# Optimization experiments

Hardware: AMD Instinct MI355X
Metric: run time of the kernel (lower is better)

Reference implementation:

```python
import math
import jax, jax.numpy as jnp
import numpy as np

HID = 256; NH = 8; DH = 32; DFF = 1024  # int(4.0*256)
N = 10000; E = 160000; NV = 128; NG = 64


def _ln(x, eps=1e-6):
    m = jnp.mean(x, axis=-1, keepdims=True)
    v = jnp.mean((x - m) ** 2, axis=-1, keepdims=True)
    return (x - m) * jax.lax.rsqrt(v + eps)


def _modulate(x, shift, scale):
    return x * (1.0 + scale) + shift


def _swiglu(x, W12, Wout):
    a, b = jnp.split(x @ W12, 2, axis=-1)
    return (jax.nn.silu(a) * b) @ Wout


def _adaln(t, W, b):
    return jnp.split(jax.nn.silu(t) @ W + b, 6, axis=-1)


def setup_inputs() -> dict:
    key = jax.random.key(0)
    ks = jax.random.split(key, 32)
    rn = lambda k, shape, s=1.0: jax.random.normal(k, shape, jnp.float32) * s
    W = 0.02
    return {
        "batch": jnp.sort(jax.random.randint(ks[0], (N,), 0, NG)),
        "x": rn(ks[1], (N, HID)),
        "t_emb_h": rn(ks[2], (N, HID)),
        "edge_attr": rn(ks[3], (E, HID)),
        "edge_index": jax.random.randint(ks[4], (2, E), 0, N),
        "t_emb_e": rn(ks[5], (E, HID)),
        "dist": rn(ks[6], (E, NV)),
        "W_edge_emb": rn(ks[7], (HID + NV, HID), W),
        "b_edge_emb": jnp.zeros((HID,), jnp.float32),
        "W_adaln": rn(ks[8], (HID, 6 * HID), W),
        "b_adaln": jnp.zeros((6 * HID,), jnp.float32),
        "W_adaln_e": rn(ks[9], (HID, 6 * HID), W),
        "b_adaln_e": jnp.zeros((6 * HID,), jnp.float32),
        "W_qkv": rn(ks[10], (HID, 3 * HID), W),
        "W_e0": rn(ks[11], (HID, HID), W),
        "W_e1": rn(ks[12], (HID, HID), W),
        "W_n2e": rn(ks[13], (HID, HID), W),
        "b_n2e": jnp.zeros((HID,), jnp.float32),
        "g_ln": jnp.ones((HID,), jnp.float32),
        "b_ln": jnp.zeros((HID,), jnp.float32),
        "W_ffn12": rn(ks[14], (HID, 2 * DFF), W),
        "W_ffn_out": rn(ks[15], (DFF, HID), W),
        "W_ffne12": rn(ks[16], (HID, 2 * DFF), W),
        "W_ffne_out": rn(ks[17], (DFF, HID), W),
    }


def reference(batch, x, t_emb_h, edge_attr, edge_index, t_emb_e, dist,
              W_edge_emb, b_edge_emb, W_adaln, b_adaln, W_adaln_e, b_adaln_e,
              W_qkv, W_e0, W_e1, W_n2e, b_n2e, g_ln, b_ln,
              W_ffn12, W_ffn_out, W_ffne12, W_ffne_out):
    src, tgt = edge_index[0], edge_index[1]
    n = x.shape[0]
    h_in_node = x
    h_in_edge = edge_attr

    shift_msa, scale_msa, gate_msa, shift_mlp, scale_mlp, gate_mlp = _adaln(t_emb_h, W_adaln, b_adaln)
    e_shift_msa, e_scale_msa, e_gate_msa, e_shift_mlp, e_scale_mlp, e_gate_mlp = _adaln(t_emb_e, W_adaln_e, b_adaln_e)

    edge_attr_e = jnp.concatenate([edge_attr, dist], axis=-1) @ W_edge_emb + b_edge_emb
    x_mod = _modulate(_ln(x), shift_msa, scale_msa)
    prev_edge_attr = edge_attr_e
    e_mod = _modulate(_ln(edge_attr_e), e_shift_msa, e_scale_msa)

    qkv = x_mod @ W_qkv                         # N x 3H
    Q, K, V = jnp.split(qkv, 3, axis=-1)
    Q = Q.reshape(-1, NH, DH)
    K = K.reshape(-1, NH, DH)
    V = V.reshape(-1, NH, DH)

    query_i = Q[src]                            # E x NH x DH
    key_j = K[tgt]
    value_j = V[tgt]
    edge_attn = jax.nn.gelu(e_mod @ W_e0, approximate=True).reshape(-1, NH, DH)

    alpha = jnp.sum(query_i * key_j * edge_attn, axis=-1) / math.sqrt(DH)  # E x NH
    # segment softmax over edges grouped by target node
    amax = jax.ops.segment_max(alpha, tgt, num_segments=n)                 # N x NH
    exp_a = jnp.exp(alpha - amax[tgt])
    denom = jax.ops.segment_sum(exp_a, tgt, num_segments=n)
    alpha = exp_a / denom[tgt]

    msg = value_j * (e_mod @ W_e1).reshape(-1, NH, DH) * alpha[..., None]
    out = jax.ops.segment_sum(msg.reshape(-1, NH * DH), tgt, num_segments=n)  # N x H

    h_node = out
    h_edge = (h_node[src] + h_node[tgt]) @ W_n2e + b_n2e

    h_node = h_in_node + gate_msa * h_node
    h_node = _modulate(_ln(h_node) * g_ln + b_ln, shift_mlp, scale_mlp)
    h_out = h_node + gate_mlp * _swiglu(h_node, W_ffn12, W_ffn_out)

    h_edge = h_in_edge + e_gate_msa * h_edge
    h_edge = _modulate(_ln(h_edge), e_shift_mlp, e_scale_mlp)
    h_edge_out = prev_edge_attr + h_edge + e_gate_mlp * _swiglu(h_edge, W_ffne12, W_ffne_out)
    return (h_out, h_edge_out)
```

## Files before the change

### kernel.cpp

```cpp
#include <hip/hip_runtime.h>

#define HID 256

typedef unsigned short u16;
typedef __attribute__((ext_vector_type(8))) short bf16x8;
typedef __attribute__((ext_vector_type(4))) float f32x4;

__device__ __forceinline__ float siluf(float x) { return x / (1.f + __expf(-x)); }
__device__ __forceinline__ float geluf(float x) {
    return x / (1.f + __expf(-(1.59576912f * x + 0.07135481f * x * x * x)));
}
__device__ __forceinline__ u16 f2b(float x) {
    unsigned u = __float_as_uint(x);
    unsigned r = u + 0x7FFFu + ((u >> 16) & 1u);
    return (u16)(r >> 16);
}
__device__ __forceinline__ float b2f(u16 h) {
    return __uint_as_float(((unsigned)h) << 16);
}
__device__ __forceinline__ void gload16(const u16* g, u16* l) {
    __builtin_amdgcn_global_load_lds(
        (const __attribute__((address_space(1))) unsigned int*)g,
        (__attribute__((address_space(3))) unsigned int*)l, 16, 0, 0);
}
__device__ __forceinline__ int imin(int a, int b) { return a < b ? a : b; }

union B16x8 { u16 u[8]; uint4 q; };

__global__ __launch_bounds__(256) void gemm_mfma(
    const u16* __restrict__ A, int lda,
    const u16* __restrict__ Bt, int ldb,
    void* __restrict__ Cv, int ldc,
    int M, int N, int K,
    const float* __restrict__ bias, int act, int obf16)
{
    __shared__ u16 lds[8192];

    const int tid  = threadIdx.x;
    const int lane = tid & 63;
    const int wave = tid >> 6;
    const int row0 = blockIdx.y * 64;
    const int col0 = blockIdx.x * 128;
    const int wm   = (wave >> 1) * 32;
    const int wn   = (wave & 1) * 64;

    f32x4 acc[2][4];
#pragma unroll
    for (int i = 0; i < 2; ++i)
#pragma unroll
        for (int j = 0; j < 4; ++j) acc[i][j] = (f32x4)0.0f;

    const int kc = (lane & 3) * 8;
    const int rr  = wave * 16 + (lane >> 2);
    const int rb1 = (wave + 4) * 16 + (lane >> 2);
    const u16* pa  = A + (size_t)imin(row0 + rr, M - 1) * lda + kc;
    const u16* pb0 = Bt + (size_t)(col0 + rr) * ldb + kc;
    const u16* pb1 = Bt + (size_t)(col0 + rb1) * ldb + kc;
    u16* la  = &lds[wave * 512];
    u16* lb0 = &lds[2048 + wave * 512];
    u16* lb1 = &lds[2048 + (wave + 4) * 512];

    const int kb = (lane >> 4) * 8;
    const int fr = lane & 15;

    for (int k0 = 0; k0 < K; k0 += 32) {
        gload16(pa + k0, la);
        gload16(pb0 + k0, lb0);
        gload16(pb1 + k0, lb1);
        __syncthreads();

        bf16x8 af[2], bfm[4];
#pragma unroll
        for (int i = 0; i < 2; ++i)
            af[i] = *(const bf16x8*)&lds[(wm + i * 16 + fr) * 32 + kb];
#pragma unroll
        for (int j = 0; j < 4; ++j)
            bfm[j] = *(const bf16x8*)&lds[2048 + (wn + j * 16 + fr) * 32 + kb];
#pragma unroll
        for (int i = 0; i < 2; ++i)
#pragma unroll
            for (int j = 0; j < 4; ++j)
                acc[i][j] = __builtin_amdgcn_mfma_f32_16x16x32_bf16(af[i], bfm[j], acc[i][j], 0, 0, 0);
        __syncthreads();
    }

    const int qr = (lane >> 4) * 4;
    if (obf16) {
#pragma unroll
        for (int i = 0; i < 2; ++i)
#pragma unroll
            for (int r = 0; r < 4; ++r)
#pragma unroll
                for (int j = 0; j < 4; ++j) {
                    int lcol = wn + j * 16 + fr;
                    int gcol = col0 + lcol;
                    float v = acc[i][j][r];
                    if (bias) v += bias[gcol];
                    if (act == 2) v = geluf(v);
                    else if (act == 1) v = siluf(v);
                    lds[(wm + i * 16 + qr + r) * 128 + lcol] = f2b(v);
                }
        __syncthreads();
        int row = tid >> 2, cc0 = (tid & 3) * 32;
        int grow = row0 + row;
        if (grow < M) {
            uint4* dst = (uint4*)((u16*)Cv + (size_t)grow * ldc + col0 + cc0);
            const uint4* sp = (const uint4*)&lds[row * 128 + cc0];
            dst[0] = sp[0]; dst[1] = sp[1]; dst[2] = sp[2]; dst[3] = sp[3];
        }
    } else {
        float* Cf = (float*)Cv;
#pragma unroll
        for (int i = 0; i < 2; ++i)
#pragma unroll
            for (int r = 0; r < 4; ++r) {
                int grow = row0 + wm + i * 16 + qr + r;
                if (grow >= M) continue;
#pragma unroll
                for (int j = 0; j < 4; ++j) {
                    int gcol = col0 + wn + j * 16 + fr;
                    float v = acc[i][j][r];
                    if (bias) v += bias[gcol];
                    if (act == 2) v = geluf(v);
                    else if (act == 1) v = siluf(v);
                    Cf[(size_t)grow * ldc + gcol] = v;
                }
            }
    }
}

__global__ __launch_bounds__(256) void gemm_e01(
    const u16* __restrict__ A, const u16* __restrict__ Bt,
    u16* __restrict__ e1b, int M,
    const u16* __restrict__ qkv, const int* __restrict__ srcI, const int* __restrict__ tgtI,
    float* __restrict__ alpha)
{
    __shared__ u16 lds[8192];

    const int tid  = threadIdx.x;
    const int lane = tid & 63;
    const int wave = tid >> 6;
    const int row0 = blockIdx.y * 64;
    const int bx   = blockIdx.x;
    const int col0 = bx * 128;
    const int wm   = (wave >> 1) * 32;
    const int wn   = (wave & 1) * 64;

    f32x4 acc[2][4];
#pragma unroll
    for (int i = 0; i < 2; ++i)
#pragma unroll
        for (int j = 0; j < 4; ++j) acc[i][j] = (f32x4)0.0f;

    const int kc = (lane & 3) * 8;
    const int rr  = wave * 16 + (lane >> 2);
    const int rb1 = (wave + 4) * 16 + (lane >> 2);
    const u16* pa  = A + (size_t)imin(row0 + rr, M - 1) * 256 + kc;
    const u16* pb0 = Bt + (size_t)(col0 + rr) * 256 + kc;
    const u16* pb1 = Bt + (size_t)(col0 + rb1) * 256 + kc;
    u16* la  = &lds[wave * 512];
    u16* lb0 = &lds[2048 + wave * 512];
    u16* lb1 = &lds[2048 + (wave + 4) * 512];

    const int kb = (lane >> 4) * 8;
    const int fr = lane & 15;

    for (int k0 = 0; k0 < 256; k0 += 32) {
        gload16(pa + k0, la);
        gload16(pb0 + k0, lb0);
        gload16(pb1 + k0, lb1);
        __syncthreads();

        bf16x8 af[2], bfm[4];
#pragma unroll
        for (int i = 0; i < 2; ++i)
            af[i] = *(const bf16x8*)&lds[(wm + i * 16 + fr) * 32 + kb];
#pragma unroll
        for (int j = 0; j < 4; ++j)
            bfm[j] = *(const bf16x8*)&lds[2048 + (wn + j * 16 + fr) * 32 + kb];
#pragma unroll
        for (int i = 0; i < 2; ++i)
#pragma unroll
            for (int j = 0; j < 4; ++j)
                acc[i][j] = __builtin_amdgcn_mfma_f32_16x16x32_bf16(af[i], bfm[j], acc[i][j], 0, 0, 0);
        __syncthreads();
    }

    const int qr = (lane >> 4) * 4;
    const bool isE0 = (bx < 2);
#pragma unroll
    for (int i = 0; i < 2; ++i)
#pragma unroll
        for (int r = 0; r < 4; ++r)
#pragma unroll
            for (int j = 0; j < 4; ++j) {
                int lcol = wn + j * 16 + fr;
                float v = acc[i][j][r];
                if (isE0) v = geluf(v);
                lds[(wm + i * 16 + qr + r) * 128 + lcol] = f2b(v);
            }
    __syncthreads();
    int row = tid >> 2, cc0 = (tid & 3) * 32;
    int grow = row0 + row;
    if (grow < M) {
        if (isE0) {
            int head = bx * 4 + (tid & 3);
            const u16* qv = qkv + (size_t)srcI[grow] * 768 + head * 32;
            const u16* kv = qkv + (size_t)tgtI[grow] * 768 + 256 + head * 32;
            const u16* gv = &lds[row * 128 + cc0];
            float s = 0.f;
#pragma unroll
            for (int c = 0; c < 32; ++c)
                s += b2f(gv[c]) * b2f(qv[c]) * b2f(kv[c]);
            alpha[(size_t)grow * 8 + head] = s * 0.17677669529663687f;
        } else {
            uint4* dst = (uint4*)(e1b + (size_t)grow * 256 + (col0 - 256) + cc0);
            const uint4* sp = (const uint4*)&lds[row * 128 + cc0];
            dst[0] = sp[0]; dst[1] = sp[1]; dst[2] = sp[2]; dst[3] = sp[3];
        }
    }
}

__global__ __launch_bounds__(256) void gemm_cat(
    const float* __restrict__ A1, const float* __restrict__ A2,
    const u16* __restrict__ Bt,
    u16* __restrict__ C, int M, const float* __restrict__ bias)
{
    __shared__ u16 lds[8192];

    const int tid  = threadIdx.x;
    const int lane = tid & 63;
    const int wave = tid >> 6;
    const int row0 = blockIdx.y * 64;
    const int col0 = blockIdx.x * 128;
    const int wm   = (wave >> 1) * 32;
    const int wn   = (wave & 1) * 64;

    f32x4 acc[2][4];
#pragma unroll
    for (int i = 0; i < 2; ++i)
#pragma unroll
        for (int j = 0; j < 4; ++j) acc[i][j] = (f32x4)0.0f;

    const int kc = (lane & 3) * 8;
    const int rr  = wave * 16 + (lane >> 2);
    const int rb1 = (wave + 4) * 16 + (lane >> 2);
    const int gr  = imin(row0 + rr, M - 1);
    const u16* pb0 = Bt + (size_t)(col0 + rr) * 384 + kc;
    const u16* pb1 = Bt + (size_t)(col0 + rb1) * 384 + kc;
    u16* lb0 = &lds[2048 + wave * 512];
    u16* lb1 = &lds[2048 + (wave + 4) * 512];
    u16* laD = &lds[wave * 512 + (lane & 63) * 8];

    const int kb = (lane >> 4) * 8;
    const int fr = lane & 15;

    for (int k0 = 0; k0 < 384; k0 += 32) {
        int kk = k0 + kc;
        const float* sp = (kk < 256) ? (A1 + (size_t)gr * 256 + kk)
                                     : (A2 + (size_t)gr * 128 + (kk - 256));
        float4 v0 = *(const float4*)sp;
        float4 v1 = *(const float4*)(sp + 4);
        gload16(pb0 + k0, lb0);
        gload16(pb1 + k0, lb1);
        B16x8 t;
        t.u[0] = f2b(v0.x); t.u[1] = f2b(v0.y); t.u[2] = f2b(v0.z); t.u[3] = f2b(v0.w);
        t.u[4] = f2b(v1.x); t.u[5] = f2b(v1.y); t.u[6] = f2b(v1.z); t.u[7] = f2b(v1.w);
        *(uint4*)laD = t.q;
        __syncthreads();

        bf16x8 af[2], bfm[4];
#pragma unroll
        for (int i = 0; i < 2; ++i)
            af[i] = *(const bf16x8*)&lds[(wm + i * 16 + fr) * 32 + kb];
#pragma unroll
        for (int j = 0; j < 4; ++j)
            bfm[j] = *(const bf16x8*)&lds[2048 + (wn + j * 16 + fr) * 32 + kb];
#pragma unroll
        for (int i = 0; i < 2; ++i)
#pragma unroll
            for (int j = 0; j < 4; ++j)
                acc[i][j] = __builtin_amdgcn_mfma_f32_16x16x32_bf16(af[i], bfm[j], acc[i][j], 0, 0, 0);
        __syncthreads();
    }

    const int qr = (lane >> 4) * 4;
#pragma unroll
    for (int i = 0; i < 2; ++i)
#pragma unroll
        for (int r = 0; r < 4; ++r)
#pragma unroll
            for (int j = 0; j < 4; ++j) {
                int lcol = wn + j * 16 + fr;
                float v = acc[i][j][r] + bias[col0 + lcol];
                lds[(wm + i * 16 + qr + r) * 128 + lcol] = f2b(v);
            }
    __syncthreads();
    int row = tid >> 2, cc0 = (tid & 3) * 32;
    int grow = row0 + row;
    if (grow < M) {
        uint4* dst = (uint4*)(C + (size_t)grow * 256 + col0 + cc0);
        const uint4* sp = (const uint4*)&lds[row * 128 + cc0];
        dst[0] = sp[0]; dst[1] = sp[1]; dst[2] = sp[2]; dst[3] = sp[3];
    }
}

__global__ __launch_bounds__(256) void gemm_gsum(
    const float* __restrict__ hat, const int* __restrict__ srcI, const int* __restrict__ tgtI,
    const u16* __restrict__ Bt,
    u16* __restrict__ C, int M, const float* __restrict__ bias)
{
    __shared__ u16 lds[8192];

    const int tid  = threadIdx.x;
    const int lane = tid & 63;
    const int wave = tid >> 6;
    const int row0 = blockIdx.y * 64;
    const int col0 = blockIdx.x * 128;
    const int wm   = (wave >> 1) * 32;
    const int wn   = (wave & 1) * 64;

    f32x4 acc[2][4];
#pragma unroll
    for (int i = 0; i < 2; ++i)
#pragma unroll
        for (int j = 0; j < 4; ++j) acc[i][j] = (f32x4)0.0f;

    const int kc = (lane & 3) * 8;
    const int rr  = wave * 16 + (lane >> 2);
    const int rb1 = (wave + 4) * 16 + (lane >> 2);
    const int gr  = imin(row0 + rr, M - 1);
    const float* ps = hat + (size_t)srcI[gr] * 256 + kc;
    const float* pt = hat + (size_t)tgtI[gr] * 256 + kc;
    const u16* pb0 = Bt + (size_t)(col0 + rr) * 256 + kc;
    const u16* pb1 = Bt + (size_t)(col0 + rb1) * 256 + kc;
    u16* lb0 = &lds[2048 + wave * 512];
    u16* lb1 = &lds[2048 + (wave + 4) * 512];
    u16* laD = &lds[wave * 512 + (lane & 63) * 8];

    const int kb = (lane >> 4) * 8;
    const int fr = lane & 15;

    for (int k0 = 0; k0 < 256; k0 += 32) {
        float4 a0 = *(const float4*)(ps + k0);
        float4 a1 = *(const float4*)(ps + k0 + 4);
        float4 b0 = *(const float4*)(pt + k0);
        float4 b1 = *(const float4*)(pt + k0 + 4);
        gload16(pb0 + k0, lb0);
        gload16(pb1 + k0, lb1);
        B16x8 t;
        t.u[0] = f2b(a0.x + b0.x); t.u[1] = f2b(a0.y + b0.y);
        t.u[2] = f2b(a0.z + b0.z); t.u[3] = f2b(a0.w + b0.w);
        t.u[4] = f2b(a1.x + b1.x); t.u[5] = f2b(a1.y + b1.y);
        t.u[6] = f2b(a1.z + b1.z); t.u[7] = f2b(a1.w + b1.w);
        *(uint4*)laD = t.q;
        __syncthreads();

        bf16x8 af[2], bfm[4];
#pragma unroll
        for (int i = 0; i < 2; ++i)
            af[i] = *(const bf16x8*)&lds[(wm + i * 16 + fr) * 32 + kb];
#pragma unroll
        for (int j = 0; j < 4; ++j)
            bfm[j] = *(const bf16x8*)&lds[2048 + (wn + j * 16 + fr) * 32 + kb];
#pragma unroll
        for (int i = 0; i < 2; ++i)
#pragma unroll
            for (int j = 0; j < 4; ++j)
                acc[i][j] = __builtin_amdgcn_mfma_f32_16x16x32_bf16(af[i], bfm[j], acc[i][j], 0, 0, 0);
        __syncthreads();
    }

    const int qr = (lane >> 4) * 4;
#pragma unroll
    for (int i = 0; i < 2; ++i)
#pragma unroll
        for (int r = 0; r < 4; ++r)
#pragma unroll
            for (int j = 0; j < 4; ++j) {
                int lcol = wn + j * 16 + fr;
                float v = acc[i][j][r] + bias[col0 + lcol];
                lds[(wm + i * 16 + qr + r) * 128 + lcol] = f2b(v);
            }
    __syncthreads();
    int row = tid >> 2, cc0 = (tid & 3) * 32;
    int grow = row0 + row;
    if (grow < M) {
        uint4* dst = (uint4*)(C + (size_t)grow * 256 + col0 + cc0);
        const uint4* sp = (const uint4*)&lds[row * 128 + cc0];
        dst[0] = sp[0]; dst[1] = sp[1]; dst[2] = sp[2]; dst[3] = sp[3];
    }
}

__global__ __launch_bounds__(256) void gemm_ffn12(
    const u16* __restrict__ A, const u16* __restrict__ Wt,
    u16* __restrict__ C, int M)
{
    __shared__ u16 sm[6144];
    u16* lsA = sm;
    u16* lsB1 = sm + 2048;
    u16* lsB2 = sm + 4096;

    const int tid  = threadIdx.x;
    const int lane = tid & 63;
    const int wave = tid >> 6;
    const int row0 = blockIdx.y * 64;
    const int col0 = blockIdx.x * 64;
    const int wm   = (wave >> 1) * 32;
    const int wn   = (wave & 1) * 32;

    f32x4 accA[2][2], accB[2][2];
#pragma unroll
    for (int i = 0; i < 2; ++i)
#pragma unroll
        for (int j = 0; j < 2; ++j) { accA[i][j] = (f32x4)0.0f; accB[i][j] = (f32x4)0.0f; }

    const int kc = (lane & 3) * 8;
    const int rr = wave * 16 + (lane >> 2);
    const u16* pa  = A + (size_t)imin(row0 + rr, M - 1) * 256 + kc;
    const u16* pb1 = Wt + (size_t)(col0 + rr) * 256 + kc;
    const u16* pb2 = Wt + (size_t)(1024 + col0 + rr) * 256 + kc;
    u16* la  = &lsA[wave * 512];
    u16* lb1 = &lsB1[wave * 512];
    u16* lb2 = &lsB2[wave * 512];

    const int kb = (lane >> 4) * 8;
    const int fr = lane & 15;

#pragma unroll 1
    for (int k0 = 0; k0 < 256; k0 += 32) {
        gload16(pa + k0, la);
        gload16(pb1 + k0, lb1);
        gload16(pb2 + k0, lb2);
        __syncthreads();

        bf16x8 af[2], b1f[2], b2f_[2];
#pragma unroll
        for (int i = 0; i < 2; ++i)
            af[i] = *(const bf16x8*)&lsA[(wm + i * 16 + fr) * 32 + kb];
#pragma unroll
        for (int j = 0; j < 2; ++j) {
            b1f[j] = *(const bf16x8*)&lsB1[(wn + j * 16 + fr) * 32 + kb];
            b2f_[j] = *(const bf16x8*)&lsB2[(wn + j * 16 + fr) * 32 + kb];
        }
#pragma unroll
        for (int i = 0; i < 2; ++i)
#pragma unroll
            for (int j = 0; j < 2; ++j) {
                accA[i][j] = __builtin_amdgcn_mfma_f32_16x16x32_bf16(af[i], b1f[j], accA[i][j], 0, 0, 0);
                accB[i][j] = __builtin_amdgcn_mfma_f32_16x16x32_bf16(af[i], b2f_[j], accB[i][j], 0, 0, 0);
            }
        __syncthreads();
    }

    const int qr = (lane >> 4) * 4;
#pragma unroll
    for (int i = 0; i < 2; ++i)
#pragma unroll
        for (int r = 0; r < 4; ++r)
#pragma unroll
            for (int j = 0; j < 2; ++j) {
                float a = accA[i][j][r], b = accB[i][j][r];
                sm[(wm + i * 16 + qr + r) * 64 + wn + j * 16 + fr] = f2b(siluf(a) * b);
            }
    __syncthreads();
    int row = tid >> 2, cc0 = (tid & 3) * 16;
    int grow = row0 + row;
    if (grow < M) {
        uint4* dst = (uint4*)(C + (size_t)grow * 1024 + col0 + cc0);
        const uint4* sp = (const uint4*)&sm[row * 64 + cc0];
        dst[0] = sp[0]; dst[1] = sp[1];
    }
}

__global__ __launch_bounds__(256) void gemm_out_final(
    const u16* __restrict__ A, const u16* __restrict__ Bt,
    const u16* __restrict__ eae, const u16* __restrict__ h2,
    const u16* __restrict__ gate, int ldg, int goff,
    float* __restrict__ out, int M)
{
    __shared__ u16 lds[6144];

    const int tid  = threadIdx.x;
    const int lane = tid & 63;
    const int wave = tid >> 6;
    const int row0 = blockIdx.y * 64;
    const int col0 = blockIdx.x * 128;
    const int wm   = (wave >> 1) * 32;
    const int wn   = (wave & 1) * 64;

    f32x4 acc[2][4];
#pragma unroll
    for (int i = 0; i < 2; ++i)
#pragma unroll
        for (int j = 0; j < 4; ++j) acc[i][j] = (f32x4)0.0f;

    const int kc = (lane & 3) * 8;
    const int rr = wave * 16 + (lane >> 2);
    const int rb1 = (wave + 4) * 16 + (lane >> 2);
    const u16* pa  = A + (size_t)imin(row0 + rr, M - 1) * 1024 + kc;
    const u16* pb0 = Bt + (size_t)(col0 + rr) * 1024 + kc;
    const u16* pb1 = Bt + (size_t)(col0 + rb1) * 1024 + kc;
    u16* la  = &lds[wave * 512];
    u16* lb0 = &lds[2048 + wave * 512];
    u16* lb1 = &lds[2048 + (wave + 4) * 512];

    const int kb = (lane >> 4) * 8;
    const int fr = lane & 15;

#pragma unroll 1
    for (int k0 = 0; k0 < 1024; k0 += 32) {
        gload16(pa + k0, la);
        gload16(pb0 + k0, lb0);
        gload16(pb1 + k0, lb1);
        __syncthreads();

        bf16x8 af[2], bfm[4];
#pragma unroll
        for (int i = 0; i < 2; ++i)
            af[i] = *(const bf16x8*)&lds[(wm + i * 16 + fr) * 32 + kb];
#pragma unroll
        for (int j = 0; j < 4; ++j)
            bfm[j] = *(const bf16x8*)&lds[2048 + (wn + j * 16 + fr) * 32 + kb];
#pragma unroll
        for (int i = 0; i < 2; ++i)
#pragma unroll
            for (int j = 0; j < 4; ++j)
                acc[i][j] = __builtin_amdgcn_mfma_f32_16x16x32_bf16(af[i], bfm[j], acc[i][j], 0, 0, 0);
        __syncthreads();
    }

    const int qr = (lane >> 4) * 4;
#pragma unroll
    for (int i = 0; i < 2; ++i)
#pragma unroll
        for (int r = 0; r < 4; ++r) {
            int grow = row0 + wm + i * 16 + qr + r;
            if (grow >= M) continue;
#pragma unroll
            for (int j = 0; j < 4; ++j) {
                int gcol = col0 + wn + j * 16 + fr;
                size_t idx = (size_t)grow * 256 + gcol;
                float v = acc[i][j][r] * b2f(gate[(size_t)grow * ldg + goff + gcol]) + b2f(h2[idx]);
                if (eae) v += b2f(eae[idx]);
                out[idx] = v;
            }
        }
}

__global__ __launch_bounds__(256) void k_wconv(
    const float* __restrict__ W, u16* __restrict__ Wt, int K, int N)
{
    int i = blockIdx.x * 256 + threadIdx.x;
    if (i >= K * N) return;
    int n = i / K, k = i - n * K;
    Wt[i] = f2b(W[(size_t)k * N + n]);
}

__global__ __launch_bounds__(256) void k_silu_b16(
    const float* __restrict__ src, u16* __restrict__ dst, long long n4)
{
    long long i = (long long)blockIdx.x * 256 + threadIdx.x;
    if (i >= n4) return;
    float4 v = ((const float4*)src)[i];
    ushort4 o;
    o.x = f2b(siluf(v.x)); o.y = f2b(siluf(v.y)); o.z = f2b(siluf(v.z)); o.w = f2b(siluf(v.w));
    ((ushort4*)dst)[i] = o;
}

__global__ __launch_bounds__(256) void k_ln_mod_b16(
    const float* __restrict__ X, u16* __restrict__ Y, int M,
    const u16* __restrict__ ssb, int ldss, int shoff, int scoff)
{
    int row = (blockIdx.x << 2) + (threadIdx.x >> 6);
    if (row >= M) return;
    int lane = threadIdx.x & 63;
    const float* xr = X + (size_t)row * HID + lane * 4;
    float x0 = xr[0], x1 = xr[1], x2 = xr[2], x3 = xr[3];
    float s = x0 + x1 + x2 + x3;
    float q = x0 * x0 + x1 * x1 + x2 * x2 + x3 * x3;
#pragma unroll
    for (int o = 32; o; o >>= 1) { s += __shfl_xor(s, o, 64); q += __shfl_xor(q, o, 64); }
    float m = s * (1.f / HID);
    float r = rsqrtf(q * (1.f / HID) - m * m + 1e-6f);
    const u16* sp = ssb + (size_t)row * ldss;
    ushort4 sh = *(const ushort4*)(sp + shoff + lane * 4);
    ushort4 sc = *(const ushort4*)(sp + scoff + lane * 4);
    ushort4 o;
    o.x = f2b((x0 - m) * r * (1.f + b2f(sc.x)) + b2f(sh.x));
    o.y = f2b((x1 - m) * r * (1.f + b2f(sc.y)) + b2f(sh.y));
    o.z = f2b((x2 - m) * r * (1.f + b2f(sc.z)) + b2f(sh.z));
    o.w = f2b((x3 - m) * r * (1.f + b2f(sc.w)) + b2f(sh.w));
    ((ushort4*)(Y + (size_t)row * HID))[lane] = o;
}

__global__ __launch_bounds__(256) void k_ln_mod_b16src(
    const u16* __restrict__ X, u16* __restrict__ Y, int M,
    const u16* __restrict__ ssb, int ldss, int shoff, int scoff)
{
    int row = (blockIdx.x << 2) + (threadIdx.x >> 6);
    if (row >= M) return;
    int lane = threadIdx.x & 63;
    ushort4 xv = ((const ushort4*)(X + (size_t)row * HID))[lane];
    float x0 = b2f(xv.x), x1 = b2f(xv.y), x2 = b2f(xv.z), x3 = b2f(xv.w);
    float s = x0 + x1 + x2 + x3;
    float q = x0 * x0 + x1 * x1 + x2 * x2 + x3 * x3;
#pragma unroll
    for (int o = 32; o; o >>= 1) { s += __shfl_xor(s, o, 64); q += __shfl_xor(q, o, 64); }
    float m = s * (1.f / HID);
    float r = rsqrtf(q * (1.f / HID) - m * m + 1e-6f);
    const u16* sp = ssb + (size_t)row * ldss;
    ushort4 sh = *(const ushort4*)(sp + shoff + lane * 4);
    ushort4 sc = *(const ushort4*)(sp + scoff + lane * 4);
    ushort4 o;
    o.x = f2b((x0 - m) * r * (1.f + b2f(sc.x)) + b2f(sh.x));
    o.y = f2b((x1 - m) * r * (1.f + b2f(sc.y)) + b2f(sh.y));
    o.z = f2b((x2 - m) * r * (1.f + b2f(sc.z)) + b2f(sh.z));
    o.w = f2b((x3 - m) * r * (1.f + b2f(sc.w)) + b2f(sh.w));
    ((ushort4*)(Y + (size_t)row * HID))[lane] = o;
}

__global__ __launch_bounds__(256) void k_ln_mod_resid_b16(
    const float* __restrict__ A, const float* __restrict__ Bv, u16* __restrict__ Y, int M,
    const u16* __restrict__ gb, int ldg, int goff,
    const u16* __restrict__ ssb, int ldss, int shoff, int scoff,
    const float* __restrict__ gw, const float* __restrict__ bw)
{
    int row = (blockIdx.x << 2) + (threadIdx.x >> 6);
    if (row >= M) return;
    int lane = threadIdx.x & 63;
    const float* ar = A + (size_t)row * HID + lane * 4;
    const float* br = Bv + (size_t)row * HID + lane * 4;
    ushort4 gp = *(const ushort4*)(gb + (size_t)row * ldg + goff + lane * 4);
    float t0 = ar[0] + b2f(gp.x) * br[0];
    float t1 = ar[1] + b2f(gp.y) * br[1];
    float t2 = ar[2] + b2f(gp.z) * br[2];
    float t3 = ar[3] + b2f(gp.w) * br[3];
    float s = t0 + t1 + t2 + t3;
    float q = t0 * t0 + t1 * t1 + t2 * t2 + t3 * t3;
#pragma unroll
    for (int o = 32; o; o >>= 1) { s += __shfl_xor(s, o, 64); q += __shfl_xor(q, o, 64); }
    float m = s * (1.f / HID);
    float r = rsqrtf(q * (1.f / HID) - m * m + 1e-6f);
    float n0 = (t0 - m) * r, n1 = (t1 - m) * r, n2 = (t2 - m) * r, n3 = (t3 - m) * r;
    if (gw) {
        const float* g4 = gw + lane * 4;
        const float* b4 = bw + lane * 4;
        n0 = n0 * g4[0] + b4[0]; n1 = n1 * g4[1] + b4[1];
        n2 = n2 * g4[2] + b4[2]; n3 = n3 * g4[3] + b4[3];
    }
    const u16* sp = ssb + (size_t)row * ldss;
    ushort4 sh = *(const ushort4*)(sp + shoff + lane * 4);
    ushort4 sc = *(const ushort4*)(sp + scoff + lane * 4);
    ushort4 o;
    o.x = f2b(n0 * (1.f + b2f(sc.x)) + b2f(sh.x));
    o.y = f2b(n1 * (1.f + b2f(sc.y)) + b2f(sh.y));
    o.z = f2b(n2 * (1.f + b2f(sc.z)) + b2f(sh.z));
    o.w = f2b(n3 * (1.f + b2f(sc.w)) + b2f(sh.w));
    ((ushort4*)(Y + (size_t)row * HID))[lane] = o;
}

__global__ __launch_bounds__(256) void k_ln_mod_resid_b16bv(
    const float* __restrict__ A, const u16* __restrict__ Bv, u16* __restrict__ Y, int M,
    const u16* __restrict__ gb, int ldg, int goff,
    const u16* __restrict__ ssb, int ldss, int shoff, int scoff)
{
    int row = (blockIdx.x << 2) + (threadIdx.x >> 6);
    if (row >= M) return;
    int lane = threadIdx.x & 63;
    const float* ar = A + (size_t)row * HID + lane * 4;
    ushort4 bv = ((const ushort4*)(Bv + (size_t)row * HID))[lane];
    ushort4 gp = *(const ushort4*)(gb + (size_t)row * ldg + goff + lane * 4);
    float t0 = ar[0] + b2f(gp.x) * b2f(bv.x);
    float t1 = ar[1] + b2f(gp.y) * b2f(bv.y);
    float t2 = ar[2] + b2f(gp.z) * b2f(bv.z);
    float t3 = ar[3] + b2f(gp.w) * b2f(bv.w);
    float s = t0 + t1 + t2 + t3;
    float q = t0 * t0 + t1 * t1 + t2 * t2 + t3 * t3;
#pragma unroll
    for (int o = 32; o; o >>= 1) { s += __shfl_xor(s, o, 64); q += __shfl_xor(q, o, 64); }
    float m = s * (1.f / HID);
    float r = rsqrtf(q * (1.f / HID) - m * m + 1e-6f);
    float n0 = (t0 - m) * r, n1 = (t1 - m) * r, n2 = (t2 - m) * r, n3 = (t3 - m) * r;
    const u16* sp = ssb + (size_t)row * ldss;
    ushort4 sh = *(const ushort4*)(sp + shoff + lane * 4);
    ushort4 sc = *(const ushort4*)(sp + scoff + lane * 4);
    ushort4 o;
    o.x = f2b(n0 * (1.f + b2f(sc.x)) + b2f(sh.x));
    o.y = f2b(n1 * (1.f + b2f(sc.y)) + b2f(sh.y));
    o.z = f2b(n2 * (1.f + b2f(sc.z)) + b2f(sh.z));
    o.w = f2b(n3 * (1.f + b2f(sc.w)) + b2f(sh.w));
    ((ushort4*)(Y + (size_t)row * HID))[lane] = o;
}

__global__ __launch_bounds__(256) void k_hist(
    const int* __restrict__ tgt, int* __restrict__ counts, int E)
{
    int i = blockIdx.x * 256 + threadIdx.x;
    if (i < E) atomicAdd(&counts[tgt[i]], 1);
}

__global__ __launch_bounds__(256) void k_scan(
    const int* __restrict__ counts, int* __restrict__ offsets, int Nn)
{
    __shared__ int part[256];
    __shared__ int pref[257];
    int t = threadIdx.x;
    int chunk = (Nn + 255) / 256;
    int lo = t * chunk, hi = imin(lo + chunk, Nn);
    int s = 0;
    for (int i = lo; i < hi; ++i) s += counts[i];
    part[t] = s;
    __syncthreads();
    if (t == 0) {
        int run = 0;
        for (int i = 0; i < 256; ++i) { pref[i] = run; run += part[i]; }
        pref[256] = run;
        offsets[Nn] = run;
    }
    __syncthreads();
    int run = pref[t];
    for (int i = lo; i < hi; ++i) { offsets[i] = run; run += counts[i]; }
}

__global__ __launch_bounds__(256) void k_scatter(
    const int* __restrict__ tgt, int* __restrict__ cursor,
    int* __restrict__ eidlist, int E)
{
    int i = blockIdx.x * 256 + threadIdx.x;
    if (i < E) {
        int pos = atomicAdd(&cursor[tgt[i]], 1);
        eidlist[pos] = i;
    }
}

__global__ __launch_bounds__(256) void k_amax_den(
    const float* __restrict__ alpha, const int* __restrict__ offsets,
    const int* __restrict__ eidlist, float* __restrict__ amaxF,
    float* __restrict__ invden, int NH8)
{
    int i = blockIdx.x * 256 + threadIdx.x;
    if (i >= NH8) return;
    int n = i >> 3, h = i & 7;
    int b = offsets[n], e = offsets[n + 1];
    float m = -1e30f;
    for (int k = b; k < e; ++k) m = fmaxf(m, alpha[(size_t)eidlist[k] * 8 + h]);
    float s = 0.f;
    for (int k = b; k < e; ++k) s += __expf(alpha[(size_t)eidlist[k] * 8 + h] - m);
    amaxF[i] = m;
    invden[i] = (s > 0.f) ? 1.f / s : 0.f;
}

__global__ __launch_bounds__(256) void k_norm(
    float* __restrict__ alpha, const float* __restrict__ amaxF,
    const float* __restrict__ invden, const int* __restrict__ tgt, int EH)
{
    int i = blockIdx.x * 256 + threadIdx.x;
    if (i >= EH) return;
    int e = i >> 3, h = i & 7;
    int g = tgt[e];
    alpha[i] = __expf(alpha[i] - amaxF[(size_t)g * 8 + h]) * invden[(size_t)g * 8 + h];
}

__global__ __launch_bounds__(256) void attn_msg_csr(
    const u16* __restrict__ qkv, const u16* __restrict__ e1b,
    const float* __restrict__ alpha, const int* __restrict__ offsets,
    const int* __restrict__ eidlist, float* __restrict__ hattn)
{
    int n = blockIdx.x;
    int c = threadIdx.x;
    int h = c >> 5;
    int b = offsets[n], e = offsets[n + 1];
    float acc = 0.f;
    for (int k = b; k < e; ++k) {
        int eid = eidlist[k];
        float w = alpha[(size_t)eid * 8 + h];
        acc += b2f(e1b[(size_t)eid * 256 + c]) * w;
    }
    hattn[(size_t)n * 256 + c] = b2f(qkv[(size_t)n * 768 + 512 + c]) * acc;
}

static inline void gemm(hipStream_t st, const u16* A, int lda, const u16* Bt, int ldb,
                        void* C, int ldc, int M, int N, int K,
                        const float* bias, int act, int obf16)
{
    dim3 g(N / 128, (M + 63) / 64);
    hipLaunchKernelGGL(gemm_mfma, g, dim3(256), 0, st, A, lda, Bt, ldb, C, ldc, M, N, K,
                       bias, act, obf16);
}

extern "C" void kernel_launch(void* const* d_in, const int* in_sizes, int n_in,
                              void* d_out, int out_size, void* d_ws, size_t ws_size,
                              hipStream_t stream)
{
    const int Nn = in_sizes[0];
    const int E = in_sizes[3] / HID;

    const float* x        = (const float*)d_in[1];
    const float* t_emb_h  = (const float*)d_in[2];
    const float* edge_attr= (const float*)d_in[3];
    const int*   eidx     = (const int*)d_in[4];
    const float* t_emb_e  = (const float*)d_in[5];
    const float* dist     = (const float*)d_in[6];
    const float* W_ee     = (const float*)d_in[7];
    const float* b_ee     = (const float*)d_in[8];
    const float* W_ad     = (const float*)d_in[9];
    const float* b_ad     = (const float*)d_in[10];
    const float* W_ade    = (const float*)d_in[11];
    const float* b_ade    = (const float*)d_in[12];
    const float* W_qkv    = (const float*)d_in[13];
    const float* W_e0     = (const float*)d_in[14];
    const float* W_e1     = (const float*)d_in[15];
    const float* W_n2e    = (const float*)d_in[16];
    const float* b_n2e    = (const float*)d_in[17];
    const float* g_ln     = (const float*)d_in[18];
    const float* b_ln     = (const float*)d_in[19];
    const float* W_f12    = (const float*)d_in[20];
    const float* W_fout   = (const float*)d_in[21];
    const float* W_fe12   = (const float*)d_in[22];
    const float* W_feout  = (const float*)d_in[23];

    const int* src = eidx;
    const int* tgt = eidx + E;

    float* outN = (float*)d_out;
    float* outE = (float*)d_out + (size_t)Nn * 256;

    char* W = (char*)d_ws;
    size_t off = 0;
    auto alloc = [&](size_t bytes) -> size_t {
        size_t o = off; off += (bytes + 255) & ~(size_t)255; return o;
    };
    float*    alpha = (float*)(W + alloc((size_t)E * 8 * 4));
    float*    amaxF = (float*)(W + alloc((size_t)Nn * 8 * 4));
    float*    invden= (float*)(W + alloc((size_t)Nn * 8 * 4));
    float*    hat   = (float*)(W + alloc((size_t)Nn * 256 * 4));
    int*      offs  = (int*)(W + alloc((size_t)(Nn + 1) * 4));
    int*      cursor= (int*)(W + alloc((size_t)Nn * 4));
    int*      eidl  = (int*)(W + alloc((size_t)E * 4));
    u16*      qkvb  = (u16*)(W + alloc((size_t)Nn * 768 * 2));
    u16*      sth   = (u16*)(W + alloc((size_t)Nn * 256 * 2));
    u16*      steb  = (u16*)(W + alloc((size_t)E * 256 * 2));
    u16*      eaeb  = (u16*)(W + alloc((size_t)E * 256 * 2));
    u16*      e1b   = (u16*)(W + alloc((size_t)E * 256 * 2));
    u16*      adnb  = (u16*)(W + alloc((size_t)Nn * 1536 * 2));
    u16*      xmb   = (u16*)(W + alloc((size_t)Nn * 256 * 2));
    u16*      h2nb  = (u16*)(W + alloc((size_t)Nn * 256 * 2));
    u16*      cnb   = (u16*)(W + alloc((size_t)Nn * 1024 * 2));
    u16* weet   = (u16*)(W + alloc((size_t)256 * 384 * 2));
    u16* wadt   = (u16*)(W + alloc((size_t)1536 * 256 * 2));
    u16* wadet  = (u16*)(W + alloc((size_t)1536 * 256 * 2));
    u16* wqkvt  = (u16*)(W + alloc((size_t)768 * 256 * 2));
    u16* we01t  = (u16*)(W + alloc((size_t)512 * 256 * 2));
    u16* wn2et  = (u16*)(W + alloc((size_t)256 * 256 * 2));
    u16* wf12t  = (u16*)(W + alloc((size_t)2048 * 256 * 2));
    u16* wfoutt = (u16*)(W + alloc((size_t)256 * 1024 * 2));
    u16* wfe12t = (u16*)(W + alloc((size_t)2048 * 256 * 2));
    u16* wfeoutt= (u16*)(W + alloc((size_t)256 * 1024 * 2));

    char* pool = W + off;
    size_t poolB = (ws_size > off) ? (ws_size - off) : 0;
    auto chunkRowsB = [&](size_t bytesPerRow, int total) -> int {
        long c = (long)(poolB / bytesPerRow);
        c = (c / 256) * 256;
        if (c < 256) c = 256;
        if (c > total) c = (long)total;
        return (int)c;
    };

    hipMemsetAsync(cursor, 0, (size_t)Nn * 4, stream);
    hipLaunchKernelGGL(k_hist, dim3((E + 255) / 256), dim3(256), 0, stream, tgt, cursor, E);
    hipLaunchKernelGGL(k_scan, dim3(1), dim3(256), 0, stream, cursor, offs, Nn);
    hipMemcpyAsync(cursor, offs, (size_t)Nn * 4, hipMemcpyDeviceToDevice, stream);
    hipLaunchKernelGGL(k_scatter, dim3((E + 255) / 256), dim3(256), 0, stream,
                       tgt, cursor, eidl, E);

    {
        struct WC { const float* w; u16* wt; int K, N; } wl[] = {
            { W_ee,    weet,   384, 256 },
            { W_ad,    wadt,   256, 1536 },
            { W_ade,   wadet,  256, 1536 },
            { W_qkv,   wqkvt,  256, 768 },
            { W_e0,    we01t,  256, 256 },
            { W_e1,    we01t + 256 * 256, 256, 256 },
            { W_n2e,   wn2et,  256, 256 },
            { W_f12,   wf12t,  256, 2048 },
            { W_fout,  wfoutt, 1024, 256 },
            { W_fe12,  wfe12t, 256, 2048 },
            { W_feout, wfeoutt,1024, 256 },
        };
        for (auto& e : wl) {
            int cnt = e.K * e.N;
            hipLaunchKernelGGL(k_wconv, dim3((cnt + 255) / 256), dim3(256), 0, stream,
                               e.w, e.wt, e.K, e.N);
        }
    }

    hipLaunchKernelGGL(k_silu_b16, dim3((unsigned)(((long long)Nn * 64 + 255) / 256)), dim3(256),
                       0, stream, t_emb_h, sth, (long long)Nn * 64);
    hipLaunchKernelGGL(k_silu_b16, dim3((unsigned)(((long long)E * 64 + 255) / 256)), dim3(256),
                       0, stream, t_emb_e, steb, (long long)E * 64);

    gemm(stream, sth, 256, wadt, 256, adnb, 1536, Nn, 1536, 256, b_ad, 0, 1);
    hipLaunchKernelGGL(k_ln_mod_b16, dim3((Nn + 3) / 4), dim3(256), 0, stream,
                       x, xmb, Nn, adnb, 1536, 0, 256);
    gemm(stream, xmb, 256, wqkvt, 256, qkvb, 768, Nn, 768, 256, nullptr, 0, 1);

    {
        int C = chunkRowsB(1024 + 512, E);
        char* p = pool;
        u16* emsb = (u16*)p; p += (size_t)C * 1024;
        u16* emod = (u16*)p;
        for (int s = 0; s < E; s += C) {
            int cc = (E - s < C) ? (E - s) : C;
            hipLaunchKernelGGL(gemm_cat, dim3(2, (cc + 63) / 64), dim3(256), 0, stream,
                               edge_attr + (size_t)s * 256, dist + (size_t)s * 128,
                               weet, eaeb + (size_t)s * 256, cc, b_ee);
            gemm(stream, steb + (size_t)s * 256, 256, wadet, 256, emsb, 512, cc, 512, 256,
                 b_ade, 0, 1);
            hipLaunchKernelGGL(k_ln_mod_b16src, dim3((cc + 3) / 4), dim3(256), 0, stream,
                               eaeb + (size_t)s * 256, emod, cc, emsb, 512, 0, 256);
            hipLaunchKernelGGL(gemm_e01, dim3(4, (cc + 63) / 64), dim3(256), 0, stream,
                               emod, we01t, e1b + (size_t)s * 256, cc,
                               qkvb, src + s, tgt + s, alpha + (size_t)s * 8);
        }
    }

    hipLaunchKernelGGL(k_amax_den, dim3((Nn * 8 + 255) / 256), dim3(256), 0, stream,
                       alpha, offs, eidl, amaxF, invden, Nn * 8);
    hipLaunchKernelGGL(k_norm, dim3((E * 8 + 255) / 256), dim3(256), 0, stream,
                       alpha, amaxF, invden, tgt, E * 8);

    hipLaunchKernelGGL(attn_msg_csr, dim3(Nn), dim3(256), 0, stream,
                       qkvb, e1b, alpha, offs, eidl, hat);

    hipLaunchKernelGGL(k_ln_mod_resid_b16, dim3((Nn + 3) / 4), dim3(256), 0, stream,
                       x, hat, h2nb, Nn, adnb, 1536, 512, adnb, 1536, 768, 1024, g_ln, b_ln);
    hipLaunchKernelGGL(gemm_ffn12, dim3(16, (Nn + 63) / 64), dim3(256), 0, stream,
                       h2nb, wf12t, cnb, Nn);
    hipLaunchKernelGGL(gemm_out_final, dim3(2, (Nn + 63) / 64), dim3(256), 0, stream,
                       cnb, wfoutt, (const u16*)nullptr, h2nb, adnb, 1536, 1280, outN, Nn);

    {
        int C = chunkRowsB(2048 + 512 + 512 + 2048, E);
        char* p = pool;
        u16*   em2b = (u16*)p;  p += (size_t)C * 2048;
        u16*   hep  = (u16*)p;  p += (size_t)C * 512;
        u16*   h2e  = (u16*)p;  p += (size_t)C * 512;
        u16*   cne  = (u16*)p;
        for (int s = 0; s < E; s += C) {
            int cc = (E - s < C) ? (E - s) : C;
            hipLaunchKernelGGL(gemm_gsum, dim3(2, (cc + 63) / 64), dim3(256), 0, stream,
                               hat, src + s, tgt + s, wn2et, hep, cc, b_n2e);
            gemm(stream, steb + (size_t)s * 256, 256, wadet + 512 * 256, 256, em2b, 1024,
                 cc, 1024, 256, b_ade + 512, 0, 1);
            hipLaunchKernelGGL(k_ln_mod_resid_b16bv, dim3((cc + 3) / 4), dim3(256), 0, stream,
                               edge_attr + (size_t)s * 256, hep, h2e, cc,
                               em2b, 1024, 0, em2b, 1024, 256, 512);
            hipLaunchKernelGGL(gemm_ffn12, dim3(16, (cc + 63) / 64), dim3(256), 0, stream,
                               h2e, wfe12t, cne, cc);
            hipLaunchKernelGGL(gemm_out_final, dim3(2, (cc + 63) / 64), dim3(256), 0, stream,
                               cne, wfeoutt, eaeb + (size_t)s * 256, h2e,
                               em2b, 1024, 768, outE + (size_t)s * 256, cc);
        }
    }
    (void)n_in; (void)out_size;
}
```

Measured before the change: 1.895 ms.

## Fuse SwiGLU up-projection and down-projection into a single FFN kernel

Measured after the change: 2.211 ms. +16.7%, slower.

```diff
diff --git a/kernel.cpp b/kernel.cpp
--- a/kernel.cpp
+++ b/kernel.cpp
@@ -392,156 +392,121 @@
     }
 }
 
-__global__ __launch_bounds__(256) void gemm_ffn12(
-    const u16* __restrict__ A, const u16* __restrict__ Wt,
-    u16* __restrict__ C, int M)
-{
-    __shared__ u16 sm[6144];
-    u16* lsA = sm;
-    u16* lsB1 = sm + 2048;
-    u16* lsB2 = sm + 4096;
+__global__ __launch_bounds__(256) void gemm_ffn_full(
+    const u16* __restrict__ A, const u16* __restrict__ W12t, const u16* __restrict__ Woutt,
+    const u16* __restrict__ eae, const u16* __restrict__ gate, int ldg, int goff,
+    float* __restrict__ out, int M)
+{
+    __shared__ u16 lds[13312];
+    u16* As = lds;
+    u16* Bs = lds + 1024;
+    u16* Ps = lds + 9216;
 
     const int tid  = threadIdx.x;
     const int lane = tid & 63;
     const int wave = tid >> 6;
-    const int row0 = blockIdx.y * 64;
-    const int col0 = blockIdx.x * 64;
-    const int wm   = (wave >> 1) * 32;
-    const int wn   = (wave & 1) * 32;
-
-    f32x4 accA[2][2], accB[2][2];
+    const int row0 = blockIdx.x * 32;
+
+    const int kc   = (lane & 3) * 8;
+    const int rstg = lane >> 2;
+    const int kb   = (lane >> 4) * 8;
+    const int fr   = lane & 15;
+    const int qr   = (lane >> 4) * 4;
+
+    f32x4 oacc[2][4];
 #pragma unroll
     for (int i = 0; i < 2; ++i)
 #pragma unroll
-        for (int j = 0; j < 2; ++j) { accA[i][j] = (f32x4)0.0f; accB[i][j] = (f32x4)0.0f; }
-
-    const int kc = (lane & 3) * 8;
-    const int rr = wave * 16 + (lane >> 2);
-    const u16* pa  = A + (size_t)imin(row0 + rr, M - 1) * 256 + kc;
-    const u16* pb1 = Wt + (size_t)(col0 + rr) * 256 + kc;
-    const u16* pb2 = Wt + (size_t)(1024 + col0 + rr) * 256 + kc;
-    u16* la  = &lsA[wave * 512];
-    u16* lb1 = &lsB1[wave * 512];
-    u16* lb2 = &lsB2[wave * 512];
-
-    const int kb = (lane >> 4) * 8;
-    const int fr = lane & 15;
-
-#pragma unroll 1
-    for (int k0 = 0; k0 < 256; k0 += 32) {
-        gload16(pa + k0, la);
-        gload16(pb1 + k0, lb1);
-        gload16(pb2 + k0, lb2);
+        for (int j = 0; j < 4; ++j) oacc[i][j] = (f32x4)0.0f;
+
+    const int arow = imin(row0 + (wave & 1) * 16 + rstg, M - 1);
+
+    for (int js = 0; js < 8; ++js) {
+        f32x4 pa[2][2], pb[2][2];
+#pragma unroll
+        for (int i = 0; i < 2; ++i)
+#pragma unroll
+            for (int j = 0; j < 2; ++j) { pa[i][j] = (f32x4)0.0f; pb[i][j] = (f32x4)0.0f; }
+
+        for (int k0 = 0; k0 < 256; k0 += 32) {
+            if (wave < 2)
+                gload16(A + (size_t)arow * 256 + k0 + kc, As + (wave & 1) * 512);
+#pragma unroll
+            for (int h = 0; h < 2; ++h) {
+                int rB = h * 64 + wave * 16 + rstg;
+                gload16(W12t + (size_t)(js * 128 + rB) * 256 + k0 + kc,
+                        Bs + (h * 64 + wave * 16) * 32);
+                gload16(W12t + (size_t)(1024 + js * 128 + rB) * 256 + k0 + kc,
+                        Bs + 4096 + (h * 64 + wave * 16) * 32);
+            }
+            __syncthreads();
+
+            bf16x8 af[2], b1f[2], b2f_[2];
+#pragma unroll
+            for (int i = 0; i < 2; ++i)
+                af[i] = *(const bf16x8*)&As[(i * 16 + fr) * 32 + kb];
+#pragma unroll
+            for (int j = 0; j < 2; ++j) {
+                b1f[j]  = *(const bf16x8*)&Bs[(wave * 32 + j * 16 + fr) * 32 + kb];
+                b2f_[j] = *(const bf16x8*)&Bs[4096 + (wave * 32 + j * 16 + fr) * 32 + kb];
+            }
+#pragma unroll
+            for (int i = 0; i < 2; ++i)
+#pragma unroll
+                for (int j = 0; j < 2; ++j) {
+                    pa[i][j] = __builtin_amdgcn_mfma_f32_16x16x32_bf16(af[i], b1f[j], pa[i][j], 0, 0, 0);
+                    pb[i][j] = __builtin_amdgcn_mfma_f32_16x16x32_bf16(af[i], b2f_[j], pb[i][j], 0, 0, 0);
+                }
+            __syncthreads();
+        }
+#pragma unroll
+        for (int i = 0; i < 2; ++i)
+#pragma unroll
+            for (int r = 0; r < 4; ++r)
+#pragma unroll
+                for (int j = 0; j < 2; ++j) {
+                    float a = pa[i][j][r], b = pb[i][j][r];
+                    Ps[(i * 16 + qr + r) * 128 + wave * 32 + j * 16 + fr] = f2b(siluf(a) * b);
+                }
         __syncthreads();
 
-        bf16x8 af[2], b1f[2], b2f_[2];
-#pragma unroll
-        for (int i = 0; i < 2; ++i)
-            af[i] = *(const bf16x8*)&lsA[(wm + i * 16 + fr) * 32 + kb];
-#pragma unroll
-        for (int j = 0; j < 2; ++j) {
-            b1f[j] = *(const bf16x8*)&lsB1[(wn + j * 16 + fr) * 32 + kb];
-            b2f_[j] = *(const bf16x8*)&lsB2[(wn + j * 16 + fr) * 32 + kb];
+        for (int k2 = 0; k2 < 128; k2 += 32) {
+#pragma unroll
+            for (int h = 0; h < 4; ++h) {
+                int rW = h * 64 + wave * 16 + rstg;
+                gload16(Woutt + (size_t)rW * 1024 + js * 128 + k2 + kc,
+                        Bs + (h * 64 + wave * 16) * 32);
+            }
+            __syncthreads();
+
+            bf16x8 pf[2], wf[4];
+#pragma unroll
+            for (int i = 0; i < 2; ++i)
+                pf[i] = *(const bf16x8*)&Ps[(i * 16 + fr) * 128 + k2 + kb];
+#pragma unroll
+            for (int j = 0; j < 4; ++j)
+                wf[j] = *(const bf16x8*)&Bs[(wave * 64 + j * 16 + fr) * 32 + kb];
+#pragma unroll
+            for (int i = 0; i < 2; ++i)
+#pragma unroll
+                for (int j = 0; j < 4; ++j)
+                    oacc[i][j] = __builtin_amdgcn_mfma_f32_16x16x32_bf16(pf[i], wf[j], oacc[i][j], 0, 0, 0);
+            __syncthreads();
         }
-#pragma unroll
-        for (int i = 0; i < 2; ++i)
-#pragma unroll
-            for (int j = 0; j < 2; ++j) {
-                accA[i][j] = __builtin_amdgcn_mfma_f32_16x16x32_bf16(af[i], b1f[j], accA[i][j], 0, 0, 0);
-                accB[i][j] = __builtin_amdgcn_mfma_f32_16x16x32_bf16(af[i], b2f_[j], accB[i][j], 0, 0, 0);
-            }
-        __syncthreads();
-    }
-
-    const int qr = (lane >> 4) * 4;
+    }
+
 #pragma unroll
     for (int i = 0; i < 2; ++i)
 #pragma unroll
-        for (int r = 0; r < 4; ++r)
-#pragma unroll
-            for (int j = 0; j < 2; ++j) {
-                float a = accA[i][j][r], b = accB[i][j][r];
-                sm[(wm + i * 16 + qr + r) * 64 + wn + j * 16 + fr] = f2b(siluf(a) * b);
-            }
-    __syncthreads();
-    int row = tid >> 2, cc0 = (tid & 3) * 16;
-    int grow = row0 + row;
-    if (grow < M) {
-        uint4* dst = (uint4*)(C + (size_t)grow * 1024 + col0 + cc0);
-        const uint4* sp = (const uint4*)&sm[row * 64 + cc0];
-        dst[0] = sp[0]; dst[1] = sp[1];
-    }
-}
-
-__global__ __launch_bounds__(256) void gemm_out_final(
-    const u16* __restrict__ A, const u16* __restrict__ Bt,
-    const u16* __restrict__ eae, const u16* __restrict__ h2,
-    const u16* __restrict__ gate, int ldg, int goff,
-    float* __restrict__ out, int M)
-{
-    __shared__ u16 lds[6144];
-
-    const int tid  = threadIdx.x;
-    const int lane = tid & 63;
-    const int wave = tid >> 6;
-    const int row0 = blockIdx.y * 64;
-    const int col0 = blockIdx.x * 128;
-    const int wm   = (wave >> 1) * 32;
-    const int wn   = (wave & 1) * 64;
-
-    f32x4 acc[2][4];
-#pragma unroll
-    for (int i = 0; i < 2; ++i)
-#pragma unroll
-        for (int j = 0; j < 4; ++j) acc[i][j] = (f32x4)0.0f;
-
-    const int kc = (lane & 3) * 8;
-    const int rr = wave * 16 + (lane >> 2);
-    const int rb1 = (wave + 4) * 16 + (lane >> 2);
-    const u16* pa  = A + (size_t)imin(row0 + rr, M - 1) * 1024 + kc;
-    const u16* pb0 = Bt + (size_t)(col0 + rr) * 1024 + kc;
-    const u16* pb1 = Bt + (size_t)(col0 + rb1) * 1024 + kc;
-    u16* la  = &lds[wave * 512];
-    u16* lb0 = &lds[2048 + wave * 512];
-    u16* lb1 = &lds[2048 + (wave + 4) * 512];
-
-    const int kb = (lane >> 4) * 8;
-    const int fr = lane & 15;
-
-#pragma unroll 1
-    for (int k0 = 0; k0 < 1024; k0 += 32) {
-        gload16(pa + k0, la);
-        gload16(pb0 + k0, lb0);
-        gload16(pb1 + k0, lb1);
-        __syncthreads();
-
-        bf16x8 af[2], bfm[4];
-#pragma unroll
-        for (int i = 0; i < 2; ++i)
-            af[i] = *(const bf16x8*)&lds[(wm + i * 16 + fr) * 32 + kb];
-#pragma unroll
-        for (int j = 0; j < 4; ++j)
-            bfm[j] = *(const bf16x8*)&lds[2048 + (wn + j * 16 + fr) * 32 + kb];
-#pragma unroll
-        for (int i = 0; i < 2; ++i)
-#pragma unroll
-            for (int j = 0; j < 4; ++j)
-                acc[i][j] = __builtin_amdgcn_mfma_f32_16x16x32_bf16(af[i], bfm[j], acc[i][j], 0, 0, 0);
-        __syncthreads();
-    }
-
-    const int qr = (lane >> 4) * 4;
-#pragma unroll
-    for (int i = 0; i < 2; ++i)
-#pragma unroll
         for (int r = 0; r < 4; ++r) {
-            int grow = row0 + wm + i * 16 + qr + r;
+            int grow = row0 + i * 16 + qr + r;
             if (grow >= M) continue;
 #pragma unroll
             for (int j = 0; j < 4; ++j) {
-                int gcol = col0 + wn + j * 16 + fr;
+                int gcol = wave * 64 + j * 16 + fr;
                 size_t idx = (size_t)grow * 256 + gcol;
-                float v = acc[i][j][r] * b2f(gate[(size_t)grow * ldg + goff + gcol]) + b2f(h2[idx]);
+                float v = oacc[i][j][r] * b2f(gate[(size_t)grow * ldg + goff + gcol])
+                        + b2f(A[idx]);
                 if (eae) v += b2f(eae[idx]);
                 out[idx] = v;
             }
@@ -846,7 +811,6 @@
     u16*      adnb  = (u16*)(W + alloc((size_t)Nn * 1536 * 2));
     u16*      xmb   = (u16*)(W + alloc((size_t)Nn * 256 * 2));
     u16*      h2nb  = (u16*)(W + alloc((size_t)Nn * 256 * 2));
-    u16*      cnb   = (u16*)(W + alloc((size_t)Nn * 1024 * 2));
     u16* weet   = (u16*)(W + alloc((size_t)256 * 384 * 2));
     u16* wadt   = (u16*)(W + alloc((size_t)1536 * 256 * 2));
     u16* wadet  = (u16*)(W + alloc((size_t)1536 * 256 * 2));
@@ -936,18 +900,16 @@
 
     hipLaunchKernelGGL(k_ln_mod_resid_b16, dim3((Nn + 3) / 4), dim3(256), 0, stream,
                        x, hat, h2nb, Nn, adnb, 1536, 512, adnb, 1536, 768, 1024, g_ln, b_ln);
-    hipLaunchKernelGGL(gemm_ffn12, dim3(16, (Nn + 63) / 64), dim3(256), 0, stream,
-                       h2nb, wf12t, cnb, Nn);
-    hipLaunchKernelGGL(gemm_out_final, dim3(2, (Nn + 63) / 64), dim3(256), 0, stream,
-                       cnb, wfoutt, (const u16*)nullptr, h2nb, adnb, 1536, 1280, outN, Nn);
+    hipLaunchKernelGGL(gemm_ffn_full, dim3((Nn + 31) / 32), dim3(256), 0, stream,
+                       h2nb, wf12t, wfoutt, (const u16*)nullptr,
+                       adnb, 1536, 1280, outN, Nn);
 
     {
-        int C = chunkRowsB(2048 + 512 + 512 + 2048, E);
+        int C = chunkRowsB(2048 + 512 + 512, E);
         char* p = pool;
         u16*   em2b = (u16*)p;  p += (size_t)C * 2048;
         u16*   hep  = (u16*)p;  p += (size_t)C * 512;
-        u16*   h2e  = (u16*)p;  p += (size_t)C * 512;
-        u16*   cne  = (u16*)p;
+        u16*   h2e  = (u16*)p;
         for (int s = 0; s < E; s += C) {
             int cc = (E - s < C) ? (E - s) : C;
             hipLaunchKernelGGL(gemm_gsum, dim3(2, (cc + 63) / 64), dim3(256), 0, stream,
@@ -957,10 +919,8 @@
             hipLaunchKernelGGL(k_ln_mod_resid_b16bv, dim3((cc + 3) / 4), dim3(256), 0, stream,
                                edge_attr + (size_t)s * 256, hep, h2e, cc,
                                em2b, 1024, 0, em2b, 1024, 256, 512);
-            hipLaunchKernelGGL(gemm_ffn12, dim3(16, (cc + 63) / 64), dim3(256), 0, stream,
-                               h2e, wfe12t, cne, cc);
-            hipLaunchKernelGGL(gemm_out_final, dim3(2, (cc + 63) / 64), dim3(256), 0, stream,
-                               cne, wfeoutt, eaeb + (size_t)s * 256, h2e,
+            hipLaunchKernelGGL(gemm_ffn_full, dim3((cc + 31) / 32), dim3(256), 0, stream,
+                               h2e, wfe12t, wfeoutt, eaeb + (size_t)s * 256,
                                em2b, 1024, 768, outE + (size_t)s * 256, cc);
         }
     }
```
